# Performance work log

Hardware: AMD Instinct MI355X
Metric: run time of the kernel (lower is better)

The kernel has to match this reference:

```python
import jax, jax.numpy as jnp
import numpy as np

NEG_INF = -jnp.inf

def _maxpool(x, kh, kw):
    ph, pw = (kh - 1) // 2, (kw - 1) // 2
    return jax.lax.reduce_window(
        x, -jnp.inf, jax.lax.max,
        window_dimensions=(1, 1, kh, kw),
        window_strides=(1, 1, 1, 1),
        padding=((0, 0), (0, 0), (ph, ph), (pw, pw)))

def soft_erode(img):
    p1 = -_maxpool(-img, 3, 1)
    p2 = -_maxpool(-img, 1, 3)
    return jnp.minimum(p1, p2)

def soft_dilate(img):
    return _maxpool(img, 3, 3)

def soft_open(img):
    return soft_dilate(soft_erode(img))

def soft_skel(img, iter_num=10):
    def body(_, carry):
        skel, img1 = carry
        opened = soft_open(img1)
        skel = skel + jax.nn.relu(img1 - opened)
        return (skel, soft_erode(img1))
    skel, _ = jax.lax.fori_loop(0, iter_num, body, (jnp.zeros_like(img), img))
    return skel

def cldice_single(pred, target, eps=1e-06):
    skel_pred = soft_skel(pred)
    skel_gt = soft_skel(target)
    tprec = (skel_pred * target).sum(axis=(2, 3)) / (skel_pred.sum(axis=(2, 3)) + eps)
    tsens = (skel_gt * pred).sum(axis=(2, 3)) / (skel_gt.sum(axis=(2, 3)) + eps)
    cl_dice = 2 * tprec * tsens / (tprec + tsens + eps)
    return cl_dice.mean()

def setup_inputs() -> dict:
    key = jax.random.key(0)
    k1, k2 = jax.random.split(key)
    B, C, H, W = 16, 2, 1024, 1024
    logits = jax.random.normal(k1, (B, C, H, W), dtype=jnp.float32)
    targets = (jax.random.uniform(k2, (B, C, H, W), dtype=jnp.float32) > 0.9).astype(jnp.float32)
    return {"logits": logits, "targets": targets}

def reference(logits, targets):
    probs = jax.nn.sigmoid(logits)
    cldice_a = cldice_single(probs[:, 0:1], targets[:, 0:1])
    cldice_v = cldice_single(probs[:, 1:2], targets[:, 1:2])
    return 1.0 - 0.5 * (cldice_a + cldice_v)
```

## Files before the change

### kernel.cpp

```cpp
#include <hip/hip_runtime.h>
#include <math.h>


#define HH 1024
#define WW 1024
#define OWN_W 104
#define VROWS 128
#define NMACRO 51

#define MOD3(x) ((((x) % 3) + 3) % 3)

__device__ __forceinline__ float2 f2s(float v) { float2 r; r.x = v; r.y = v; return r; }
__device__ __forceinline__ float sigm(float x) { return __builtin_amdgcn_rcpf(1.0f + __expf(-x)); }

__device__ __forceinline__ float vmin3(float a, float b, float c) {
    float d; asm("v_min3_f32 %0, %1, %2, %3" : "=v"(d) : "v"(a), "v"(b), "v"(c)); return d;
}
__device__ __forceinline__ float vmax3(float a, float b, float c) {
    float d; asm("v_max3_f32 %0, %1, %2, %3" : "=v"(d) : "v"(a), "v"(b), "v"(c)); return d;
}
__device__ __forceinline__ float vmax(float a, float b) {
    float d; asm("v_max_f32 %0, %1, %2" : "=v"(d) : "v"(a), "v"(b)); return d;
}
__device__ __forceinline__ float relu(float x) {
    float d; asm("v_max_f32 %0, 0, %1" : "=v"(d) : "v"(x)); return d;
}
__device__ __forceinline__ float min5(float a, float b, float c, float d, float e) {
    return vmin3(vmin3(a, b, c), d, e);
}

__device__ __forceinline__ float dpp_up1(float x) {
    int i = __builtin_bit_cast(int, x);
    int r = __builtin_amdgcn_update_dpp(i, i, 0x138, 0xf, 0xf, false);
    return __builtin_bit_cast(float, r);
}
__device__ __forceinline__ float dpp_dn1(float x) {
    int i = __builtin_bit_cast(int, x);
    int r = __builtin_amdgcn_update_dpp(i, i, 0x130, 0xf, 0xf, false);
    return __builtin_bit_cast(float, r);
}

__global__ __launch_bounds__(256, 4)
void skel_kernel(const float* __restrict__ logits,
                 const float* __restrict__ targets,
                 float* __restrict__ sums)
{
    const int lane = threadIdx.x & 63;
    const int gwid = __builtin_amdgcn_readfirstlane(blockIdx.x * 4 + (threadIdx.x >> 6));
    const int job  = gwid / 80;
    const int rem  = gwid - job * 80;
    const int s    = rem % 10;
    const int v    = rem / 10;
    const int tensor = job >> 5;
    const int plane  = job & 31;
    const size_t planeOff = (size_t)plane * (HH * WW);
    const float* __restrict__ src  = tensor ? targets : logits;
    const float* __restrict__ osrc = tensor ? logits  : targets;
    const bool sEdge = (s == 0) || (s == 9);

    const int colBase = OWN_W * s - 12 + lane * 2;
    const bool colOOB = (colBase < 0) || (colBase > WW - 2);
    const int colC = colBase < 0 ? 0 : (colBase > WW - 2 ? WW - 2 : colBase);
    const int y0 = v * VROWS;
    const int rBase = y0 - 11;

    const int ownHi = (OWN_W * (s + 1) < WW) ? OWN_W * (s + 1) : WW;
    const bool ownedLane = (colBase >= OWN_W * s) && (colBase < ownHi);

    float2 E[11][3];
#pragma unroll
    for (int k = 0; k < 11; ++k)
#pragma unroll
        for (int j = 0; j < 3; ++j) E[k][j] = f2s(INFINITY);

    float2 oring[15];
#pragma unroll
    for (int j = 0; j < 15; ++j) oring[j] = f2s(0.f);

    float2 sumS = f2s(0.f), sumP = f2s(0.f);

    auto loadImg = [&](int row) -> float2 {
        float2 x;
        if ((unsigned)row < HH) {
            const float* p = src + planeOff + (size_t)row * WW + colC;
            x = *(const float2*)p;
            if (!tensor) { x.x = sigm(x.x); x.y = sigm(x.y); }
            if (sEdge && colOOB) x = f2s(INFINITY);
        } else {
            x = f2s(INFINITY);
        }
        return x;
    };
    auto loadOther = [&](int row) -> float2 {
        int rc = row < 0 ? 0 : (row > HH - 1 ? HH - 1 : row);
        const float* p = osrc + planeOff + (size_t)rc * WW + colC;
        float2 x = *(const float2*)p;
        if (tensor) { x.x = sigm(x.x); x.y = sigm(x.y); }
        return x;
    };

    float2 nextImg = loadImg(rBase);

#pragma unroll 1
    for (int m = 0; m < NMACRO; ++m) {
#pragma unroll
        for (int j = 0; j < 12; ++j) oring[j] = oring[j + 3];
#pragma unroll
        for (int j = 0; j < 3; ++j) oring[12 + j] = loadOther(rBase + 3 * m + j);

#pragma unroll
        for (int p = 0; p < 3; ++p) {
            const int r = rBase + 3 * m + p;
            const float2 img = nextImg;
            nextImg = loadImg(r + 1);

#pragma unroll
            for (int k = 1; k <= 10; ++k) {
                const int yd = r - k - 2;
                if (yd >= y0 && yd < y0 + VROWS) {
                    const float2 a = E[k][MOD3(p - k)];
                    const float2 b = E[k][MOD3(p - k + 1)];
                    const float2 c = E[k][MOD3(p - k + 2)];
                    float2 vm;
                    if (yd == 0) {
                        vm.x = vmax(b.x, c.x); vm.y = vmax(b.y, c.y);
                    } else if (yd == HH - 1) {
                        vm.x = vmax(a.x, b.x); vm.y = vmax(a.y, b.y);
                    } else {
                        vm.x = vmax3(a.x, b.x, c.x); vm.y = vmax3(a.y, b.y, c.y);
                    }
                    if (sEdge) { if (colOOB) vm = f2s(-INFINITY); }
                    const float vl = dpp_up1(vm.y);
                    const float vr = dpp_dn1(vm.x);
                    float2 h;
                    h.x = vmax3(vl,   vm.x, vm.y);
                    h.y = vmax3(vm.x, vm.y, vr);
                    const float2 io = E[k - 1][MOD3(p - k + 1)];
                    float2 ct;
                    ct.x = relu(io.x - h.x);
                    ct.y = relu(io.y - h.y);
                    const float2 ot = oring[10 + p - k];
                    sumS.x += ct.x; sumS.y += ct.y;
                    sumP.x = fmaf(ot.x, ct.x, sumP.x);
                    sumP.y = fmaf(ot.y, ct.y, sumP.y);
                }
            }

            E[0][MOD3(p)] = img;
            float2 np_ = img;
#pragma unroll
            for (int k = 1; k <= 10; ++k) {
                const float2 A = E[k - 1][MOD3(p - k + 2)];
                const float2 B = E[k - 1][MOD3(p - k)];
                const float2 C = np_;
                const float bl = dpp_up1(B.y);
                const float br = dpp_dn1(B.x);
                float2 ne;
                ne.x = min5(A.x, C.x, bl,  B.y, B.x);
                ne.y = min5(A.y, C.y, B.x, br,  B.y);
                const int yN = r - k;
                if ((unsigned)yN >= HH) {
                    ne = f2s(INFINITY);
                } else if (sEdge) {
                    if (colOOB) ne = f2s(INFINITY);
                }
                E[k][MOD3(p - k)] = ne;
                np_ = ne;
            }
        }
    }

    if (!ownedLane) { sumS = f2s(0.f); sumP = f2s(0.f); }
    float aS = sumS.x + sumS.y;
    float aP = sumP.x + sumP.y;
#pragma unroll
    for (int off = 32; off > 0; off >>= 1) {
        aS += __shfl_down(aS, off, 64);
        aP += __shfl_down(aP, off, 64);
    }
    if (lane == 0) {
        const int base = plane * 4 + tensor * 2;
        atomicAdd(&sums[base],     aS);
        atomicAdd(&sums[base + 1], aP);
    }
}

__global__ void finalize_kernel(const float* __restrict__ s4, float* __restrict__ out)
{
    __shared__ float cl[32];
    int p = threadIdx.x;
    if (p < 32) {
        const float* s = s4 + p * 4;
        float tprec = s[1] / (s[0] + 1e-6f);
        float tsens = s[3] / (s[2] + 1e-6f);
        cl[p] = 2.f * tprec * tsens / (tprec + tsens + 1e-6f);
    }
    __syncthreads();
    if (p == 0) {
        float a = 0.f, vch = 0.f;
        for (int b = 0; b < 16; ++b) { a += cl[b * 2]; vch += cl[b * 2 + 1]; }
        out[0] = 1.f - 0.5f * (a / 16.f + vch / 16.f);
    }
}

extern "C" void kernel_launch(void* const* d_in, const int* in_sizes, int n_in,
                              void* d_out, int out_size, void* d_ws, size_t ws_size,
                              hipStream_t stream)
{
    const float* logits  = (const float*)d_in[0];
    const float* targets = (const float*)d_in[1];
    float* out  = (float*)d_out;
    float* sums = (float*)d_ws;

    hipMemsetAsync(d_ws, 0, 32 * 4 * sizeof(float), stream);

    skel_kernel<<<1280, 256, 0, stream>>>(logits, targets, sums);
    finalize_kernel<<<1, 64, 0, stream>>>(sums, out);
}
```

Baseline: 730.3 us.

## Move other-tensor row ring to LDS and raise occupancy to five blocks

The 15-row register ring of the other tensor's rows is moved into per-wave shared memory, indexed through a compile-time modulo-15 slot, so the per-macro-step register shifts disappear. The macro loop is unrolled by five using template constants so all ring indices stay static. Launch bounds are raised from 4 to 5 blocks per CU, relying on the lower register pressure. The cost is extra LDS reads and writes in the inner loop and a larger unrolled body, which may increase instruction-cache pressure.

Result: slower. 878.0 us (+20.2%).

```diff
diff --git a/kernel.cpp b/kernel.cpp
--- a/kernel.cpp
+++ b/kernel.cpp
@@ -6,9 +6,12 @@
 #define WW 1024
 #define OWN_W 104
 #define VROWS 128
-#define NMACRO 51
+#define NMB 10
 
 #define MOD3(x) ((((x) % 3) + 3) % 3)
+#define MOD15(x) ((((x) % 15) + 15) % 15)
+
+template<int V> struct Int { static constexpr int value = V; };
 
 __device__ __forceinline__ float2 f2s(float v) { float2 r; r.x = v; r.y = v; return r; }
 __device__ __forceinline__ float sigm(float x) { return __builtin_amdgcn_rcpf(1.0f + __expf(-x)); }
@@ -40,13 +43,14 @@
     return __builtin_bit_cast(float, r);
 }
 
-__global__ __launch_bounds__(256, 4)
+__global__ __launch_bounds__(256, 5)
 void skel_kernel(const float* __restrict__ logits,
                  const float* __restrict__ targets,
                  float* __restrict__ sums)
 {
     const int lane = threadIdx.x & 63;
-    const int gwid = __builtin_amdgcn_readfirstlane(blockIdx.x * 4 + (threadIdx.x >> 6));
+    const int wv   = threadIdx.x >> 6;
+    const int gwid = __builtin_amdgcn_readfirstlane(blockIdx.x * 4 + wv);
     const int job  = gwid / 80;
     const int rem  = gwid - job * 80;
     const int s    = rem % 10;
@@ -61,7 +65,8 @@
     const int colBase = OWN_W * s - 12 + lane * 2;
     const bool colOOB = (colBase < 0) || (colBase > WW - 2);
     const int colC = colBase < 0 ? 0 : (colBase > WW - 2 ? WW - 2 : colBase);
-    const int y0 = v * VROWS;
+    const int y0  = v * VROWS;
+    const int yHi = y0 + VROWS;
     const int rBase = y0 - 11;
 
     const int ownHi = (OWN_W * (s + 1) < WW) ? OWN_W * (s + 1) : WW;
@@ -73,9 +78,8 @@
 #pragma unroll
         for (int j = 0; j < 3; ++j) E[k][j] = f2s(INFINITY);
 
-    float2 oring[15];
-#pragma unroll
-    for (int j = 0; j < 15; ++j) oring[j] = f2s(0.f);
+    __shared__ float oring[4][15][128];
+    float* const ringBase = &oring[wv][0][lane * 2];
 
     float2 sumS = f2s(0.f), sumP = f2s(0.f);
 
@@ -100,13 +104,16 @@
     };
 
     float2 nextImg = loadImg(rBase);
-
-#pragma unroll 1
-    for (int m = 0; m < NMACRO; ++m) {
-#pragma unroll
-        for (int j = 0; j < 12; ++j) oring[j] = oring[j + 3];
-#pragma unroll
-        for (int j = 0; j < 3; ++j) oring[12 + j] = loadOther(rBase + 3 * m + j);
+    int m = 0;
+
+    auto macroBody = [&](auto icI) {
+        constexpr int I = decltype(icI)::value;
+
+#pragma unroll
+        for (int j = 0; j < 3; ++j) {
+            float2 o = loadOther(rBase + 3 * m + j);
+            *(float2*)(ringBase + ((3 * I + j) % 15) * 128) = o;
+        }
 
 #pragma unroll
         for (int p = 0; p < 3; ++p) {
@@ -117,7 +124,7 @@
 #pragma unroll
             for (int k = 1; k <= 10; ++k) {
                 const int yd = r - k - 2;
-                if (yd >= y0 && yd < y0 + VROWS) {
+                if (yd >= y0 && yd < yHi) {
                     const float2 a = E[k][MOD3(p - k)];
                     const float2 b = E[k][MOD3(p - k + 1)];
                     const float2 c = E[k][MOD3(p - k + 2)];
@@ -139,7 +146,8 @@
                     float2 ct;
                     ct.x = relu(io.x - h.x);
                     ct.y = relu(io.y - h.y);
-                    const float2 ot = oring[10 + p - k];
+                    const float2 ot =
+                        *(const float2*)(ringBase + MOD15(3 * I + p - 2 - k) * 128);
                     sumS.x += ct.x; sumS.y += ct.y;
                     sumP.x = fmaf(ot.x, ct.x, sumP.x);
                     sumP.y = fmaf(ot.y, ct.y, sumP.y);
@@ -168,7 +176,18 @@
                 np_ = ne;
             }
         }
-    }
+        ++m;
+    };
+
+#pragma unroll 1
+    for (int mb = 0; mb < NMB; ++mb) {
+        macroBody(Int<0>{});
+        macroBody(Int<1>{});
+        macroBody(Int<2>{});
+        macroBody(Int<3>{});
+        macroBody(Int<4>{});
+    }
+    macroBody(Int<0>{});
 
     if (!ownedLane) { sumS = f2s(0.f); sumP = f2s(0.f); }
     float aS = sumS.x + sumS.y;
```
